# Kernel tuning notes

Measured on AMD Instinct MI355X. Metric: run time of the kernel, lower is better.

The kernel has to match this reference:

```python
import jax, jax.numpy as jnp
import numpy as np

B, T, C = 256, 256, 147
BPM, H_DIM, NH = 32, 64, 4
HD = H_DIM // NH


def setup_inputs() -> dict:
    key = jax.random.key(0)
    ks = jax.random.split(key, 12)
    def lin(k, fan_in, fan_out):
        bound = 1.0 / np.sqrt(fan_in)
        kw, kb = jax.random.split(k)
        W = jax.random.uniform(kw, (fan_in, fan_out), jnp.float32, -bound, bound)
        b = jax.random.uniform(kb, (fan_out,), jnp.float32, -bound, bound)
        return W, b
    Wq, bq = lin(ks[0], C, H_DIM)
    Wk, bk = lin(ks[1], C, H_DIM)
    Wv, bv = lin(ks[2], C, H_DIM)
    Wb, bb = lin(ks[3], BPM, H_DIM)
    Wo, bo = lin(ks[4], H_DIM, C)
    pose = jax.random.normal(ks[5], (B, T, C), jnp.float32)
    bpm_emb = jax.random.normal(ks[6], (B, BPM), jnp.float32)
    return {"pose": pose, "bpm_emb": bpm_emb,
            "Wq": Wq, "bq": bq, "Wk": Wk, "bk": bk, "Wv": Wv, "bv": bv,
            "Wb": Wb, "bb": bb, "Wo": Wo, "bo": bo}


def reference(pose, bpm_emb, Wq, bq, Wk, bk, Wv, bv, Wb, bb, Wo, bo):
    Bb, Tt, Cc = pose.shape
    scale = HD ** -0.5
    # projections -> [B, H, T, hd]
    def split_heads(x):
        return x.reshape(Bb, Tt, NH, HD).transpose(0, 2, 1, 3)
    q = split_heads(pose @ Wq + bq)
    k = split_heads(pose @ Wk + bk)
    v = split_heads(pose @ Wv + bv)
    # bpm-conditioned key bias: [B, H, 1, hd]
    bpm_feat = (bpm_emb @ Wb + bb).reshape(Bb, 1, NH, HD).transpose(0, 2, 1, 3)
    k = k + bpm_feat
    # attention
    scores = jnp.einsum('bhqd,bhkd->bhqk', q, k) * scale
    attn = jax.nn.softmax(scores, axis=-1)
    out = jnp.einsum('bhqk,bhkd->bhqd', attn, v)
    out = out.transpose(0, 2, 1, 3).reshape(Bb, Tt, NH * HD)
    return out @ Wo + bo
```

## Files before the change

### kernel.cpp

```cpp
#include <hip/hip_runtime.h>

constexpr int kC = 147, kH = 64, kBPM = 32;

typedef __attribute__((ext_vector_type(8)))  short bf16x8;
typedef __attribute__((ext_vector_type(4)))  float f32x4;
typedef __attribute__((ext_vector_type(16))) float f32x16;
typedef __attribute__((ext_vector_type(2)))  unsigned u32x2;
typedef __attribute__((ext_vector_type(4)))  unsigned u32x4;

__device__ __forceinline__ short f2bf(float f) {
    unsigned u = __builtin_bit_cast(unsigned, f);
    u += 0x7fffu + ((u >> 16) & 1u);
    return (short)(u >> 16);
}
__device__ __forceinline__ unsigned cvt_pk(float lo, float hi) {
    unsigned r;
    asm("v_cvt_pk_bf16_f32 %0, %1, %2" : "=v"(r) : "v"(lo), "v"(hi));
    return r;
}
#define MFMA16(a,b,c) __builtin_amdgcn_mfma_f32_16x16x32_bf16((a),(b),(c),0,0,0)
#define MFMA32(a,b,c) __builtin_amdgcn_mfma_f32_32x32x16_bf16((a),(b),(c),0,0,0)

#if __has_builtin(__builtin_amdgcn_exp2f)
  #define EXP2(x) __builtin_amdgcn_exp2f(x)
#else
  #define EXP2(x) __expf((x) * 0.6931471805599453f)
#endif
constexpr float kQScale = 0.25f * 1.4426950408889634f;

constexpr int QS  = 72;
constexpr int VS  = 264;
constexpr int PS  = 40;
constexpr int WSS = 168;
constexpr int WOS = 72;

__device__ __forceinline__ void stage_w_regs(const float* wr ,
                                             short* Ws, int tid) {
    #pragma unroll
    for (int it = 0; it < 5; ++it) {
        const int i = it * 1024 + tid;
        const int c = i & 63, k = (i >> 6) * 2;
        *(unsigned*)&Ws[c * WSS + (k ^ (((c >> 3) & 3) << 3))]
            = cvt_pk(wr[2*it], wr[2*it + 1]);
    }
}

__global__ __launch_bounds__(1024, 4) void fused_kernel(
    const float* __restrict__ pose, const float* __restrict__ bpm_emb,
    const float* __restrict__ Wq, const float* __restrict__ bq,
    const float* __restrict__ Wk, const float* __restrict__ bk,
    const float* __restrict__ Wv, const float* __restrict__ bv,
    const float* __restrict__ Wb, const float* __restrict__ bb,
    const float* __restrict__ Wo, const float* __restrict__ bo,
    float* __restrict__ out)
{
    __shared__ __align__(16) short qs[256 * QS];
    __shared__ __align__(16) short ks_[256 * QS];
    __shared__ __align__(16) short vt[kH * VS];
    __shared__ __align__(16) short WsPt[20480];
    __shared__ float l_s[16 * 64];
    __shared__ float bias_s[192];
    short* const Ws = WsPt;
    short* const Pt = WsPt;

    const int tid = threadIdx.x;
    const int w = tid >> 6, lane = tid & 63;
    const int ll = lane & 15, lq = lane >> 4;
    const int lm = lane & 31, lh = lane >> 5;
    const int b = blockIdx.x;
    const size_t pbase = (size_t)b * 256 * kC;

    float wq_r[10], wk_r[10], wv_r[10];
    #pragma unroll
    for (int it = 0; it < 5; ++it) {
        const int i = it * 1024 + tid;
        const int c = i & 63, k = (i >> 6) * 2;
        const bool b0 = k < kC, b1 = k + 1 < kC;
        wq_r[2*it]   = b0 ? Wq[k * kH + c] * kQScale : 0.f;
        wq_r[2*it+1] = b1 ? Wq[(k + 1) * kH + c] * kQScale : 0.f;
        wk_r[2*it]   = b0 ? Wk[k * kH + c] : 0.f;
        wk_r[2*it+1] = b1 ? Wk[(k + 1) * kH + c] : 0.f;
        wv_r[2*it]   = b0 ? Wv[k * kH + c] : 0.f;
        wv_r[2*it+1] = b1 ? Wv[(k + 1) * kH + c] : 0.f;
    }

    bf16x8 pf[5];
    {
        const int row = w * 16 + ll;
        const float* prow = pose + pbase + (size_t)row * kC;
        #pragma unroll
        for (int ksp = 0; ksp < 5; ++ksp) {
            const int c0 = ksp * 32 + lq * 8;
            float v[8];
            if (c0 + 8 <= kC) {
                const float4 f0 = *(const float4*)(prow + c0);
                const float4 f1 = *(const float4*)(prow + c0 + 4);
                v[0]=f0.x; v[1]=f0.y; v[2]=f0.z; v[3]=f0.w;
                v[4]=f1.x; v[5]=f1.y; v[6]=f1.z; v[7]=f1.w;
            } else {
                #pragma unroll
                for (int e = 0; e < 8; ++e) v[e] = (c0 + e < kC) ? prow[c0 + e] : 0.f;
            }
            const u32x4 t = { cvt_pk(v[0], v[1]), cvt_pk(v[2], v[3]),
                              cvt_pk(v[4], v[5]), cvt_pk(v[6], v[7]) };
            pf[ksp] = __builtin_bit_cast(bf16x8, t);
        }
    }
    if (tid < 192) {
        const int m = tid >> 6, c = tid & 63;
        float a = ((m == 0) ? bq : (m == 1) ? bk : bv)[c];
        if (m == 1) {
            a += bb[c];
            #pragma unroll
            for (int k2 = 0; k2 < kBPM; ++k2)
                a = fmaf(bpm_emb[b * kBPM + k2], Wb[k2 * kH + c], a);
        }
        if (m == 0) a *= kQScale;
        bias_s[tid] = a;
    }
    stage_w_regs(wq_r, Ws, tid);
    __syncthreads();

    #pragma unroll
    for (int m = 0; m < 3; ++m) {
        f32x4 acc[4];
        #pragma unroll
        for (int mt = 0; mt < 4; ++mt) acc[mt] = (f32x4){0.f,0.f,0.f,0.f};
        #pragma unroll
        for (int ksp = 0; ksp < 5; ++ksp)
            #pragma unroll
            for (int mt = 0; mt < 4; ++mt) {
                const int c = mt * 16 + ll;
                const int key = ((c >> 3) & 3) << 3;
                const bf16x8 wf = *(const bf16x8*)(Ws + c * WSS + ((ksp*32 + lq*8) ^ key));
                acc[mt] = MFMA16(wf, pf[ksp], acc[mt]);
            }
        __syncthreads();
        if (m == 0)      stage_w_regs(wk_r, Ws, tid);
        else if (m == 1) stage_w_regs(wv_r, Ws, tid);
        const int row = w * 16 + ll;
        #pragma unroll
        for (int mt = 0; mt < 4; ++mt) {
            const int c0 = mt * 16 + 4 * lq;
            const float4 bv4 = *(const float4*)&bias_s[m * kH + c0];
            if (m < 2) {
                const u32x2 pk = { cvt_pk(acc[mt][0] + bv4.x, acc[mt][1] + bv4.y),
                                   cvt_pk(acc[mt][2] + bv4.z, acc[mt][3] + bv4.w) };
                *(u32x2*)((m == 0 ? qs : ks_) + row * QS + c0) = pk;
            } else {
                vt[(c0 + 0) * VS + row] = f2bf(acc[mt][0] + bv4.x);
                vt[(c0 + 1) * VS + row] = f2bf(acc[mt][1] + bv4.y);
                vt[(c0 + 2) * VS + row] = f2bf(acc[mt][2] + bv4.z);
                vt[(c0 + 3) * VS + row] = f2bf(acc[mt][3] + bv4.w);
            }
        }
        __syncthreads();
    }

    const int h = w & 3;
    const int q0 = (w >> 2) * 64;
    bf16x8 qf[2];
    #pragma unroll
    for (int s32 = 0; s32 < 2; ++s32)
        qf[s32] = *(const bf16x8*)(qs + (q0 + s32*32 + lm) * QS + h*16 + lh*8);

    float wo_r[10];
    #pragma unroll
    for (int it = 0; it < 5; ++it) {
        const int i = it * 1024 + tid;
        const int n = i % 160, k = (i / 160) * 2;
        wo_r[2*it]   = (n < kC) ? Wo[k * kC + n] : 0.f;
        wo_r[2*it+1] = (n < kC) ? Wo[(k + 1) * kC + n] : 0.f;
    }

    f32x4 oacc[2][2];
    #pragma unroll
    for (int s32 = 0; s32 < 2; ++s32) {
        oacc[s32][0] = (f32x4){0.f,0.f,0.f,0.f};
        oacc[s32][1] = (f32x4){0.f,0.f,0.f,0.f};
    }
    float lp[2] = {0.f, 0.f};
    short* Pw = Pt + w * 32 * PS;
    const int wkey = ((lm >> 3) & 3) << 3;

    #pragma unroll 2
    for (int jb = 0; jb < 8; ++jb) {
        const int j0 = jb * 32;
        const bf16x8 kf = *(const bf16x8*)(ks_ + (j0 + lm) * QS + h*16 + lh*8);
        const bf16x8 vf = *(const bf16x8*)(vt + (h*16 + ll) * VS + j0 + lq*8);
        #pragma unroll
        for (int s32 = 0; s32 < 2; ++s32) {
            const f32x16 z16 = {0.f,0.f,0.f,0.f,0.f,0.f,0.f,0.f,
                                0.f,0.f,0.f,0.f,0.f,0.f,0.f,0.f};
            const f32x16 s = MFMA32(kf, qf[s32], z16);
            float sum = 0.f;
            #pragma unroll
            for (int g = 0; g < 4; ++g) {
                const float p0 = EXP2(s[4*g + 0]);
                const float p1 = EXP2(s[4*g + 1]);
                const float p2 = EXP2(s[4*g + 2]);
                const float p3 = EXP2(s[4*g + 3]);
                sum += (p0 + p1) + (p2 + p3);
                const u32x2 pk = { cvt_pk(p0, p1), cvt_pk(p2, p3) };
                *(u32x2*)(Pw + lm * PS + ((8*g + 4*lh) ^ wkey)) = pk;
            }
            lp[s32] += sum;
            #pragma unroll
            for (int half = 0; half < 2; ++half) {
                const int qp = half * 16 + ll;
                const int rkey = ((qp >> 3) & 3) << 3;
                const bf16x8 pfr = *(const bf16x8*)(Pw + qp * PS + ((lq*8) ^ rkey));
                oacc[s32][half] = MFMA16(vf, pfr, oacc[s32][half]);
            }
        }
    }
    #pragma unroll
    for (int s32 = 0; s32 < 2; ++s32) {
        const float l2 = lp[s32] + __shfl_xor(lp[s32], 32);
        if (lane < 32) l_s[w * 64 + s32 * 32 + lm] = l2;
    }
    #pragma unroll
    for (int s32 = 0; s32 < 2; ++s32)
        #pragma unroll
        for (int half = 0; half < 2; ++half) {
            const int qi = s32 * 32 + half * 16 + ll;
            const float inv = 1.f / l_s[w * 64 + qi];
            const u32x2 pk = { cvt_pk(oacc[s32][half][0] * inv, oacc[s32][half][1] * inv),
                               cvt_pk(oacc[s32][half][2] * inv, oacc[s32][half][3] * inv) };
            *(u32x2*)(qs + (q0 + qi) * QS + h*16 + 4*lq) = pk;
        }
    __syncthreads();

    #pragma unroll
    for (int it = 0; it < 5; ++it) {
        const int i = it * 1024 + tid;
        const int n = i % 160, k = (i / 160) * 2;
        *(unsigned*)&Ws[n * WOS + (k ^ (((n >> 3) & 3) << 3))]
            = cvt_pk(wo_r[2*it], wo_r[2*it + 1]);
    }
    __syncthreads();

    bf16x8 xf[2];
    #pragma unroll
    for (int k2 = 0; k2 < 2; ++k2)
        xf[k2] = *(const bf16x8*)(qs + (w*16 + ll) * QS + k2*32 + lq*8);

    f32x4 po[10];
    #pragma unroll
    for (int mt = 0; mt < 10; ++mt) po[mt] = (f32x4){0.f,0.f,0.f,0.f};
    #pragma unroll
    for (int k2 = 0; k2 < 2; ++k2)
        #pragma unroll
        for (int mt = 0; mt < 10; ++mt) {
            const int n = mt * 16 + ll;
            const int key = ((n >> 3) & 3) << 3;
            const bf16x8 wf = *(const bf16x8*)(Ws + n * WOS + ((k2*32 + lq*8) ^ key));
            po[mt] = MFMA16(wf, xf[k2], po[mt]);
        }
    {
        const int row = w * 16 + ll;
        float* orow = out + ((size_t)b * 256 + row) * kC;
        #pragma unroll
        for (int mt = 0; mt < 10; ++mt) {
            const int c0 = mt * 16 + 4 * lq;
            if (mt < 9) {
                const float4 bv4 = *(const float4*)(bo + c0);
                float4 o;
                o.x = po[mt][0] + bv4.x; o.y = po[mt][1] + bv4.y;
                o.z = po[mt][2] + bv4.z; o.w = po[mt][3] + bv4.w;
                *(float4*)(orow + c0) = o;
            } else {
                #pragma unroll
                for (int r = 0; r < 4; ++r) {
                    const int c = c0 + r;
                    if (c < kC) orow[c] = po[mt][r] + bo[c];
                }
            }
        }
    }
}

extern "C" void kernel_launch(void* const* d_in, const int* in_sizes, int n_in,
                              void* d_out, int out_size, void* d_ws, size_t ws_size,
                              hipStream_t stream) {
    const float* pose    = (const float*)d_in[0];
    const float* bpm_emb = (const float*)d_in[1];
    const float* Wq = (const float*)d_in[2];  const float* bq = (const float*)d_in[3];
    const float* Wk = (const float*)d_in[4];  const float* bk = (const float*)d_in[5];
    const float* Wv = (const float*)d_in[6];  const float* bv = (const float*)d_in[7];
    const float* Wb = (const float*)d_in[8];  const float* bb = (const float*)d_in[9];
    const float* Wo = (const float*)d_in[10]; const float* bo = (const float*)d_in[11];
    float* out = (float*)d_out;

    fused_kernel<<<256, 1024, 0, stream>>>(
        pose, bpm_emb, Wq, bq, Wk, bk, Wv, bv, Wb, bb, Wo, bo, out);
}
```

Before: 129.1 us.

## Keep softmax probabilities in registers via permlane32 swap for PV MFMA

The P tile no longer goes through a shared-memory round trip. Probabilities stay in registers, are rearranged with v_permlane32_swap, and feed 32x32x16 MFMAs for the PV product, which also lets the row-sum normalisation happen in registers without the l_s shared buffer. Wo loading and staging move earlier, into the projection phase, which removes one barrier and shrinks the shared buffer. The cost is more live registers for the early wo_r preload.

```diff
diff --git a/kernel.cpp b/kernel.cpp
--- a/kernel.cpp
+++ b/kernel.cpp
@@ -30,7 +30,6 @@
 
 constexpr int QS  = 72;
 constexpr int VS  = 264;
-constexpr int PS  = 40;
 constexpr int WSS = 168;
 constexpr int WOS = 72;
 
@@ -57,11 +56,8 @@
     __shared__ __align__(16) short qs[256 * QS];
     __shared__ __align__(16) short ks_[256 * QS];
     __shared__ __align__(16) short vt[kH * VS];
-    __shared__ __align__(16) short WsPt[20480];
-    __shared__ float l_s[16 * 64];
+    __shared__ __align__(16) short Ws[11520];
     __shared__ float bias_s[192];
-    short* const Ws = WsPt;
-    short* const Pt = WsPt;
 
     const int tid = threadIdx.x;
     const int w = tid >> 6, lane = tid & 63;
@@ -70,7 +66,7 @@
     const int b = blockIdx.x;
     const size_t pbase = (size_t)b * 256 * kC;
 
-    float wq_r[10], wk_r[10], wv_r[10];
+    float wq_r[10], wk_r[10], wv_r[10], wo_r[10];
     #pragma unroll
     for (int it = 0; it < 5; ++it) {
         const int i = it * 1024 + tid;
@@ -82,6 +78,9 @@
         wk_r[2*it+1] = b1 ? Wk[(k + 1) * kH + c] : 0.f;
         wv_r[2*it]   = b0 ? Wv[k * kH + c] : 0.f;
         wv_r[2*it+1] = b1 ? Wv[(k + 1) * kH + c] : 0.f;
+        const int n = i % 160, ko = (i / 160) * 2;
+        wo_r[2*it]   = (n < kC) ? Wo[ko * kC + n] : 0.f;
+        wo_r[2*it+1] = (n < kC) ? Wo[(ko + 1) * kC + n] : 0.f;
     }
 
     bf16x8 pf[5];
@@ -138,6 +137,15 @@
         __syncthreads();
         if (m == 0)      stage_w_regs(wk_r, Ws, tid);
         else if (m == 1) stage_w_regs(wv_r, Ws, tid);
+        else {
+            #pragma unroll
+            for (int it = 0; it < 5; ++it) {
+                const int i = it * 1024 + tid;
+                const int n = i % 160, k = (i / 160) * 2;
+                *(unsigned*)&Ws[n * WOS + (k ^ (((n >> 3) & 3) << 3))]
+                    = cvt_pk(wo_r[2*it], wo_r[2*it + 1]);
+            }
+        }
         const int row = w * 16 + ll;
         #pragma unroll
         for (int mt = 0; mt < 4; ++mt) {
@@ -164,36 +172,27 @@
     for (int s32 = 0; s32 < 2; ++s32)
         qf[s32] = *(const bf16x8*)(qs + (q0 + s32*32 + lm) * QS + h*16 + lh*8);
 
-    float wo_r[10];
-    #pragma unroll
-    for (int it = 0; it < 5; ++it) {
-        const int i = it * 1024 + tid;
-        const int n = i % 160, k = (i / 160) * 2;
-        wo_r[2*it]   = (n < kC) ? Wo[k * kC + n] : 0.f;
-        wo_r[2*it+1] = (n < kC) ? Wo[(k + 1) * kC + n] : 0.f;
-    }
-
-    f32x4 oacc[2][2];
-    #pragma unroll
-    for (int s32 = 0; s32 < 2; ++s32) {
-        oacc[s32][0] = (f32x4){0.f,0.f,0.f,0.f};
-        oacc[s32][1] = (f32x4){0.f,0.f,0.f,0.f};
-    }
+    f32x16 oacc[2];
+    #pragma unroll
+    for (int s32 = 0; s32 < 2; ++s32)
+        oacc[s32] = (f32x16){0.f,0.f,0.f,0.f,0.f,0.f,0.f,0.f,
+                             0.f,0.f,0.f,0.f,0.f,0.f,0.f,0.f};
     float lp[2] = {0.f, 0.f};
-    short* Pw = Pt + w * 32 * PS;
-    const int wkey = ((lm >> 3) & 3) << 3;
+    const int vrow = h * 16 + (lm & 15);
+    const f32x16 z16 = {0.f,0.f,0.f,0.f,0.f,0.f,0.f,0.f,
+                        0.f,0.f,0.f,0.f,0.f,0.f,0.f,0.f};
 
     #pragma unroll 2
     for (int jb = 0; jb < 8; ++jb) {
         const int j0 = jb * 32;
-        const bf16x8 kf = *(const bf16x8*)(ks_ + (j0 + lm) * QS + h*16 + lh*8);
-        const bf16x8 vf = *(const bf16x8*)(vt + (h*16 + ll) * VS + j0 + lq*8);
+        const bf16x8 kf  = *(const bf16x8*)(ks_ + (j0 + lm) * QS + h*16 + lh*8);
+        const bf16x8 va0 = *(const bf16x8*)(vt + vrow * VS + j0 + lh*8);
+        const bf16x8 va1 = *(const bf16x8*)(vt + vrow * VS + j0 + 16 + lh*8);
         #pragma unroll
         for (int s32 = 0; s32 < 2; ++s32) {
-            const f32x16 z16 = {0.f,0.f,0.f,0.f,0.f,0.f,0.f,0.f,
-                                0.f,0.f,0.f,0.f,0.f,0.f,0.f,0.f};
             const f32x16 s = MFMA32(kf, qf[s32], z16);
             float sum = 0.f;
+            unsigned u[8];
             #pragma unroll
             for (int g = 0; g < 4; ++g) {
                 const float p0 = EXP2(s[4*g + 0]);
@@ -201,42 +200,33 @@
                 const float p2 = EXP2(s[4*g + 2]);
                 const float p3 = EXP2(s[4*g + 3]);
                 sum += (p0 + p1) + (p2 + p3);
-                const u32x2 pk = { cvt_pk(p0, p1), cvt_pk(p2, p3) };
-                *(u32x2*)(Pw + lm * PS + ((8*g + 4*lh) ^ wkey)) = pk;
+                u[2*g]   = cvt_pk(p0, p1);
+                u[2*g+1] = cvt_pk(p2, p3);
             }
             lp[s32] += sum;
-            #pragma unroll
-            for (int half = 0; half < 2; ++half) {
-                const int qp = half * 16 + ll;
-                const int rkey = ((qp >> 3) & 3) << 3;
-                const bf16x8 pfr = *(const bf16x8*)(Pw + qp * PS + ((lq*8) ^ rkey));
-                oacc[s32][half] = MFMA16(vf, pfr, oacc[s32][half]);
-            }
+            unsigned a0 = u[0], a1 = u[1], b0 = u[2], b1 = u[3];
+            asm("v_permlane32_swap_b32 %0, %1" : "+v"(a0), "+v"(b0));
+            asm("v_permlane32_swap_b32 %0, %1" : "+v"(a1), "+v"(b1));
+            unsigned c0 = u[4], c1 = u[5], d0 = u[6], d1 = u[7];
+            asm("v_permlane32_swap_b32 %0, %1" : "+v"(c0), "+v"(d0));
+            asm("v_permlane32_swap_b32 %0, %1" : "+v"(c1), "+v"(d1));
+            const u32x4 pb0 = { a0, a1, b0, b1 };
+            const u32x4 pb1 = { c0, c1, d0, d1 };
+            oacc[s32] = MFMA32(va0, __builtin_bit_cast(bf16x8, pb0), oacc[s32]);
+            oacc[s32] = MFMA32(va1, __builtin_bit_cast(bf16x8, pb1), oacc[s32]);
         }
     }
     #pragma unroll
     for (int s32 = 0; s32 < 2; ++s32) {
         const float l2 = lp[s32] + __shfl_xor(lp[s32], 32);
-        if (lane < 32) l_s[w * 64 + s32 * 32 + lm] = l2;
-    }
-    #pragma unroll
-    for (int s32 = 0; s32 < 2; ++s32)
-        #pragma unroll
-        for (int half = 0; half < 2; ++half) {
-            const int qi = s32 * 32 + half * 16 + ll;
-            const float inv = 1.f / l_s[w * 64 + qi];
-            const u32x2 pk = { cvt_pk(oacc[s32][half][0] * inv, oacc[s32][half][1] * inv),
-                               cvt_pk(oacc[s32][half][2] * inv, oacc[s32][half][3] * inv) };
-            *(u32x2*)(qs + (q0 + qi) * QS + h*16 + 4*lq) = pk;
-        }
-    __syncthreads();
-
-    #pragma unroll
-    for (int it = 0; it < 5; ++it) {
-        const int i = it * 1024 + tid;
-        const int n = i % 160, k = (i / 160) * 2;
-        *(unsigned*)&Ws[n * WOS + (k ^ (((n >> 3) & 3) << 3))]
-            = cvt_pk(wo_r[2*it], wo_r[2*it + 1]);
+        const float inv = 1.f / l2;
+        const int row = q0 + s32 * 32 + lm;
+        const u32x2 pkA = { cvt_pk(oacc[s32][0] * inv, oacc[s32][1] * inv),
+                            cvt_pk(oacc[s32][2] * inv, oacc[s32][3] * inv) };
+        *(u32x2*)(qs + row * QS + h*16 + 4*lh) = pkA;
+        const u32x2 pkB = { cvt_pk(oacc[s32][4] * inv, oacc[s32][5] * inv),
+                            cvt_pk(oacc[s32][6] * inv, oacc[s32][7] * inv) };
+        *(u32x2*)(qs + row * QS + h*16 + 8 + 4*lh) = pkB;
     }
     __syncthreads();
 
```

Result: slower. 132.0 us (+2.2%).

## Double-buffer QKV weight staging in LDS to cut barriers and register pressure

Applied to the files above, without the earlier changes.

The kernel now splits the weight staging area into two LDS buffers, so the next projection's weights (K, then V) are written while the current projection's MFMAs read the other buffer. The K/V weight global loads are deferred and interleaved with compute instead of all being loaded up front. This removes one barrier per projection and lowers live register count, which matters under launch_bounds(1024,4). In exchange the shared buffer grows slightly, and the reordered loads may expose more global-load latency.

```diff
diff --git a/kernel.cpp b/kernel.cpp
--- a/kernel.cpp
+++ b/kernel.cpp
@@ -57,11 +57,13 @@
     __shared__ __align__(16) short qs[256 * QS];
     __shared__ __align__(16) short ks_[256 * QS];
     __shared__ __align__(16) short vt[kH * VS];
-    __shared__ __align__(16) short WsPt[20480];
+    __shared__ __align__(16) short WsPt[21504];
     __shared__ float l_s[16 * 64];
     __shared__ float bias_s[192];
-    short* const Ws = WsPt;
-    short* const Pt = WsPt;
+    short* const WsA = WsPt;
+    short* const WsB = WsPt + 10752;
+    short* const Pt  = WsPt;
+    short* const Ws  = WsPt;
 
     const int tid = threadIdx.x;
     const int w = tid >> 6, lane = tid & 63;
@@ -69,20 +71,6 @@
     const int lm = lane & 31, lh = lane >> 5;
     const int b = blockIdx.x;
     const size_t pbase = (size_t)b * 256 * kC;
-
-    float wq_r[10], wk_r[10], wv_r[10];
-    #pragma unroll
-    for (int it = 0; it < 5; ++it) {
-        const int i = it * 1024 + tid;
-        const int c = i & 63, k = (i >> 6) * 2;
-        const bool b0 = k < kC, b1 = k + 1 < kC;
-        wq_r[2*it]   = b0 ? Wq[k * kH + c] * kQScale : 0.f;
-        wq_r[2*it+1] = b1 ? Wq[(k + 1) * kH + c] * kQScale : 0.f;
-        wk_r[2*it]   = b0 ? Wk[k * kH + c] : 0.f;
-        wk_r[2*it+1] = b1 ? Wk[(k + 1) * kH + c] : 0.f;
-        wv_r[2*it]   = b0 ? Wv[k * kH + c] : 0.f;
-        wv_r[2*it+1] = b1 ? Wv[(k + 1) * kH + c] : 0.f;
-    }
 
     bf16x8 pf[5];
     {
@@ -106,6 +94,14 @@
             pf[ksp] = __builtin_bit_cast(bf16x8, t);
         }
     }
+    float wq_r[10];
+    #pragma unroll
+    for (int it = 0; it < 5; ++it) {
+        const int i = it * 1024 + tid;
+        const int c = i & 63, k = (i >> 6) * 2;
+        wq_r[2*it]   = (k     < kC) ? Wq[k * kH + c] * kQScale : 0.f;
+        wq_r[2*it+1] = (k + 1 < kC) ? Wq[(k + 1) * kH + c] * kQScale : 0.f;
+    }
     if (tid < 192) {
         const int m = tid >> 6, c = tid & 63;
         float a = ((m == 0) ? bq : (m == 1) ? bk : bv)[c];
@@ -118,12 +114,10 @@
         if (m == 0) a *= kQScale;
         bias_s[tid] = a;
     }
-    stage_w_regs(wq_r, Ws, tid);
+    stage_w_regs(wq_r, WsA, tid);
     __syncthreads();
 
-    #pragma unroll
-    for (int m = 0; m < 3; ++m) {
-        f32x4 acc[4];
+    auto qkv_mfma = [&](const short* R, f32x4 (&acc)[4]) {
         #pragma unroll
         for (int mt = 0; mt < 4; ++mt) acc[mt] = (f32x4){0.f,0.f,0.f,0.f};
         #pragma unroll
@@ -132,12 +126,11 @@
             for (int mt = 0; mt < 4; ++mt) {
                 const int c = mt * 16 + ll;
                 const int key = ((c >> 3) & 3) << 3;
-                const bf16x8 wf = *(const bf16x8*)(Ws + c * WSS + ((ksp*32 + lq*8) ^ key));
+                const bf16x8 wf = *(const bf16x8*)(R + c * WSS + ((ksp*32 + lq*8) ^ key));
                 acc[mt] = MFMA16(wf, pf[ksp], acc[mt]);
             }
-        __syncthreads();
-        if (m == 0)      stage_w_regs(wk_r, Ws, tid);
-        else if (m == 1) stage_w_regs(wv_r, Ws, tid);
+    };
+    auto qkv_epi = [&](const f32x4 (&acc)[4], int m) {
         const int row = w * 16 + ll;
         #pragma unroll
         for (int mt = 0; mt < 4; ++mt) {
@@ -154,6 +147,41 @@
                 vt[(c0 + 3) * VS + row] = f2bf(acc[mt][3] + bv4.w);
             }
         }
+    };
+
+    {
+        float wk_r[10];
+        #pragma unroll
+        for (int it = 0; it < 5; ++it) {
+            const int i = it * 1024 + tid;
+            const int c = i & 63, k = (i >> 6) * 2;
+            wk_r[2*it]   = (k     < kC) ? Wk[k * kH + c] : 0.f;
+            wk_r[2*it+1] = (k + 1 < kC) ? Wk[(k + 1) * kH + c] : 0.f;
+        }
+        f32x4 acc[4];
+        qkv_mfma(WsA, acc);
+        stage_w_regs(wk_r, WsB, tid);
+        float wv_r[10];
+        #pragma unroll
+        for (int it = 0; it < 5; ++it) {
+            const int i = it * 1024 + tid;
+            const int c = i & 63, k = (i >> 6) * 2;
+            wv_r[2*it]   = (k     < kC) ? Wv[k * kH + c] : 0.f;
+            wv_r[2*it+1] = (k + 1 < kC) ? Wv[(k + 1) * kH + c] : 0.f;
+        }
+        qkv_epi(acc, 0);
+        __syncthreads();
+
+        f32x4 acc1[4];
+        qkv_mfma(WsB, acc1);
+        stage_w_regs(wv_r, WsA, tid);
+        qkv_epi(acc1, 1);
+        __syncthreads();
+    }
+    {
+        f32x4 acc[4];
+        qkv_mfma(WsA, acc);
+        qkv_epi(acc, 2);
         __syncthreads();
     }
 
```

Measured after the change: 147.5 us. +14.3%, slower.
